# Kernel optimization log

Hardware: AMD Instinct MI355X
Metric: run time of the kernel (lower is better)

## Reference

```python
import jax, jax.numpy as jnp
import numpy as np

EPS = 1e-12  # torch F.normalize default eps


def conv1x1(x, w, b):
    # x: [N,C,H,W], w: [K,C], b: [K]
    return jnp.einsum('nchw,kc->nkhw', x, w) + b[None, :, None, None]


def forward_sa(f1, f2, cw1, cb1, cw2, cb2):
    n, _, h, w = f1.shape
    c1 = conv1x1(f1, cw1, cb1)  # [N,1,H,W]
    c2 = conv1x1(f2, cw2, cb2)
    c1 = jax.nn.softmax(c1.reshape(n, h * w), axis=1).reshape(n, 1, h, w)
    c2 = jax.nn.softmax(c2.reshape(n, h * w), axis=1).reshape(n, 1, h, w)
    return c1 * f1, c2 * f2


def l2norm_ch(x):
    # torch F.normalize(x) -> p=2 over dim=1 with eps clamp
    n = jnp.sqrt(jnp.sum(x * x, axis=1, keepdims=True))
    return x / jnp.maximum(n, EPS)


def forward_ca(f1, f2, pw1, pb1, pw2, pb2):
    N, C, H, W = f1.shape
    f1_cl = conv1x1(f1, pw1, pb1).reshape(N, -1, H * W)  # [N,Cl,HW]
    f2_cl = conv1x1(f2, pw2, pb2).reshape(N, -1, H * W)
    # A[n,p,q] = sum_c f2_cl[n,c,p] * f1_cl[n,c,q]  -> [N,HW,HW]
    A_c = jnp.tanh(jnp.einsum('ncp,ncq->npq', f2_cl, f1_cl))
    f1_v = f1.reshape(N, C, H * W)
    f2_v = f2.reshape(N, C, H * W)
    # f1_hat = f1_v @ A_c^T ; f2_hat = f2_v @ A_c
    f1_hat = jnp.einsum('ncp,nqp->ncq', f1_v, A_c).reshape(N, C, H, W)
    f2_hat = jnp.einsum('ncp,npq->ncq', f2_v, A_c).reshape(N, C, H, W)
    return l2norm_ch(f1_hat), l2norm_ch(f2_hat)


def setup_inputs() -> dict:
    key = jax.random.key(0)
    ks = jax.random.split(key, 10)
    N, C, H, W = 2, 256, 64, 64
    Cl = C // 16
    sc = 1.0 / np.sqrt(C)
    return {
        'f1': jax.random.normal(ks[0], (N, C, H, W), jnp.float32),
        'f2': jax.random.normal(ks[1], (N, C, H, W), jnp.float32),
        'pw1': jax.random.normal(ks[2], (Cl, C), jnp.float32) * sc,
        'pb1': jax.random.normal(ks[3], (Cl,), jnp.float32) * sc,
        'pw2': jax.random.normal(ks[4], (Cl, C), jnp.float32) * sc,
        'pb2': jax.random.normal(ks[5], (Cl,), jnp.float32) * sc,
        'cw1': jax.random.normal(ks[6], (1, C), jnp.float32) * sc,
        'cb1': jax.random.normal(ks[7], (1,), jnp.float32) * sc,
        'cw2': jax.random.normal(ks[8], (1, C), jnp.float32) * sc,
        'cb2': jax.random.normal(ks[9], (1,), jnp.float32) * sc,
    }


def reference(f1, f2, pw1, pb1, pw2, pb2, cw1, cb1, cw2, cb2):
    f1_1, f2_1 = forward_sa(f1, f2, cw1, cb1, cw2, cb2)
    f1_hat, f2_hat = forward_ca(f1_1, f2_1, pw1, pb1, pw2, pb2)
    fp1_hat = jax.nn.relu(f1_hat + f1)
    fp2_hat = jax.nn.relu(f2_hat + f2)
    f1_2, f2_2 = forward_sa(fp1_hat, fp2_hat, cw1, cb1, cw2, cb2)
    # Original calls forward_ca(f1_2, f2_2) again but discards the result
    # and returns (f1_2, f2_2); the dead call is omitted (identical output).
    return (f1_2, f2_2)
```

## Files before the change

kernel.cpp:

```cpp
#include <hip/hip_runtime.h>
#include <hip/hip_bf16.h>
#include <math.h>

#define N_B 2
#define C_CH 256
#define HW_SZ 4096
#define CL_CH 16

typedef __bf16 bf16x8 __attribute__((ext_vector_type(8)));
typedef float f32x4 __attribute__((ext_vector_type(4)));
typedef float f32x16 __attribute__((ext_vector_type(16)));

__device__ __forceinline__ unsigned short f2bf(float x){
  __hip_bfloat16 b = __float2bfloat16(x);
  return *reinterpret_cast<unsigned short*>(&b);
}
__device__ __forceinline__ unsigned int cvtpk(float a, float b){
  unsigned int r;
  asm("v_cvt_pk_bf16_f32 %0, %1, %2" : "=v"(r) : "v"(a), "v"(b));
  return r;
}
__device__ __forceinline__ float tanh_fast(float x){
  float e = __expf(2.0f * x);
  return fmaf(-2.0f, __builtin_amdgcn_rcpf(1.0f + e), 1.0f);
}
__device__ __forceinline__ void gload16(const void* gsrc, void* lds_dst){
  __builtin_amdgcn_global_load_lds(
      (const __attribute__((address_space(1))) unsigned int*)gsrc,
      (__attribute__((address_space(3))) unsigned int*)lds_dst, 16, 0, 0);
}

__global__ void k_conv1(const float* __restrict__ f1, const float* __restrict__ f2,
                        const float* __restrict__ w1, const float* __restrict__ w2,
                        const float* __restrict__ b1, const float* __restrict__ b2,
                        float* __restrict__ cv){
  const int i = blockIdx.z, n = blockIdx.y, t = threadIdx.x;
  const int ql = t & 63, cg = t >> 6;
  const int q = blockIdx.x * 64 + ql;
  const float* f = (i ? f2 : f1) + n * C_CH * HW_SZ;
  const float* w = i ? w2 : w1;
  __shared__ float ws[C_CH];
  __shared__ float red[4][72];
  ws[t] = w[t];
  __syncthreads();
  float acc = 0.f;
  #pragma unroll 8
  for (int c = cg * 64; c < cg * 64 + 64; ++c)
    acc += f[c * HW_SZ + q] * ws[c];
  red[cg][ql] = acc;
  __syncthreads();
  if (t < 64){
    float s = red[0][t] + red[1][t] + red[2][t] + red[3][t] + (i ? b2[0] : b1[0]);
    cv[(i * 2 + n) * HW_SZ + blockIdx.x * 64 + t] = s;
  }
}

__global__ void k_softmax(const float* __restrict__ cv, float* __restrict__ pr){
  const int r = blockIdx.x, t = threadIdx.x;
  const float* x = cv + r * HW_SZ;
  float* y = pr + r * HW_SZ;
  __shared__ float red[256];
  float v[16];
  float m = -1e30f;
  #pragma unroll
  for (int j = 0; j < 16; j++){ v[j] = x[j * 256 + t]; m = fmaxf(m, v[j]); }
  red[t] = m; __syncthreads();
  for (int s = 128; s > 0; s >>= 1){ if (t < s) red[t] = fmaxf(red[t], red[t + s]); __syncthreads(); }
  m = red[0]; __syncthreads();
  float sum = 0.f;
  #pragma unroll
  for (int j = 0; j < 16; j++){ v[j] = __expf(v[j] - m); sum += v[j]; }
  red[t] = sum; __syncthreads();
  for (int s = 128; s > 0; s >>= 1){ if (t < s) red[t] += red[t + s]; __syncthreads(); }
  const float inv = 1.0f / red[0];
  #pragma unroll
  for (int j = 0; j < 16; j++) y[j * 256 + t] = v[j] * inv;
}

__global__ void k_scale_cl(const float* __restrict__ f1, const float* __restrict__ f2,
                           const float* __restrict__ pr,
                           const float* __restrict__ pw1, const float* __restrict__ pw2,
                           const float* __restrict__ pb1, const float* __restrict__ pb2,
                           unsigned short* __restrict__ fs1, unsigned short* __restrict__ fs2,
                           unsigned short* __restrict__ clT1, unsigned short* __restrict__ clT2){
  const int i = blockIdx.z, n = blockIdx.y, t = threadIdx.x;
  const int ql = t & 63, cg = t >> 6;
  const int q = blockIdx.x * 64 + ql;
  const float* f = (i ? f2 : f1) + n * C_CH * HW_SZ;
  unsigned short* fs = (i ? fs2 : fs1) + n * C_CH * HW_SZ;
  unsigned short* clT = (i ? clT2 : clT1) + n * 32 * HW_SZ;
  const float* pw = i ? pw2 : pw1;
  const float* pb = i ? pb2 : pb1;
  __shared__ float wls[CL_CH * C_CH];
  __shared__ float red[4][CL_CH][66];
  #pragma unroll
  for (int j = 0; j < 16; j++) wls[j * 256 + t] = pw[j * 256 + t];
  __syncthreads();
  const float p = pr[(i * 2 + n) * HW_SZ + q];
  float acc[16];
  #pragma unroll
  for (int k = 0; k < 16; k++) acc[k] = 0.f;
  for (int c = cg * 64; c < cg * 64 + 64; ++c){
    float vv = f[c * HW_SZ + q] * p;
    fs[c * HW_SZ + q] = f2bf(vv);
    #pragma unroll
    for (int k = 0; k < 16; k++) acc[k] += wls[k * 256 + c] * vv;
  }
  #pragma unroll
  for (int k = 0; k < 16; k++) red[cg][k][ql] = acc[k];
  __syncthreads();
  #pragma unroll
  for (int j = 0; j < 4; j++){
    int e = j * 256 + t; int k = e >> 6, qq = e & 63;
    float s = red[0][k][qq] + red[1][k][qq] + red[2][k][qq] + red[3][k][qq] + pb[k];
    clT[(blockIdx.x * 64 + qq) * 32 + k] = f2bf(s);
  }
  if (t < 128){
    uint4 zv = {0u, 0u, 0u, 0u};
    int qq = t >> 1, half = t & 1;
    *reinterpret_cast<uint4*>(&clT[(blockIdx.x * 64 + qq) * 32 + 16 + half * 8]) = zv;
  }
}

__global__ __launch_bounds__(512, 4) void k_hat(
    const unsigned short* __restrict__ fs1, const unsigned short* __restrict__ fs2,
    const unsigned short* __restrict__ clT1, const unsigned short* __restrict__ clT2,
    float* __restrict__ hat1, float* __restrict__ hat2,
    float* __restrict__ pt1, float* __restrict__ pt2){
  const int t = threadIdx.x;
  const int bid = blockIdx.x;
  const int xcd = bid & 7, slot = bid >> 3;
  const int z = xcd >> 1;
  const int n = z & 1, i = z >> 1;
  const int x = slot * 2 + (xcd & 1);
  const int qt = x >> 1, ph = x & 1;
  const int q0 = qt * 64;
  const int pbase = ph * 2048;

  const unsigned short* fs = (i ? fs2 : fs1) + n * C_CH * HW_SZ;
  const unsigned short* uT = (i ? clT1 : clT2) + n * 32 * HW_SZ;
  const unsigned short* vT = (i ? clT2 : clT1) + n * 32 * HW_SZ;
  float* out = (ph ? (i ? pt2 : pt1) : (i ? hat2 : hat1)) + n * C_CH * HW_SZ;

  __shared__ __align__(16) unsigned short fsA[2][C_CH * 64];
  __shared__ __align__(16) unsigned short aT[2][64 * 64];

  const int wv = t >> 6, l = t & 63;
  const int g4 = l >> 4, lr16 = l & 15;
  const int g2 = l >> 5, lr32 = l & 31;

  const int pfw = wv & 3;
  const int qf0 = (wv >> 2) * 2;
  const int cblk = wv & 3, qblk = wv >> 2;

  const bf16x8 ub0 = *reinterpret_cast<const bf16x8*>(&uT[(q0 + qf0 * 16 + lr16) * 32 + g4 * 8]);
  const bf16x8 ub1 = *reinterpret_cast<const bf16x8*>(&uT[(q0 + qf0 * 16 + 16 + lr16) * 32 + g4 * 8]);

  f32x16 acc0, acc1;
  #pragma unroll
  for (int r = 0; r < 16; ++r){ acc0[r] = 0.f; acc1[r] = 0.f; }
  const f32x4 zz = {0.f, 0.f, 0.f, 0.f};

  int fs_src[4];
  #pragma unroll
  for (int it = 0; it < 4; ++it){
    int d = it * 512 + t; int c = d >> 3, sl = d & 7;
    int u = sl ^ (c & 7) ^ (((c >> 3) & 1) << 2);
    fs_src[it] = c * (HW_SZ * 2) + u * 16;
  }
  const char* vbase = (const char*)vT;
  const int vgo = (pfw * 16 + lr16) * 64 + g4 * 16;
  unsigned atw0;
  {
    int qd = qf0 * 16 + lr16;
    int sw = (pfw * 2 + (g4 >> 1)) ^ (qd & 7) ^ (((qd >> 3) & 1) << 2);
    atw0 = qd * 128 + sw * 16 + (g4 & 1) * 8;
  }
  unsigned afo[2], bqo;
  #pragma unroll
  for (int cf = 0; cf < 2; ++cf){
    int crow = cblk * 64 + cf * 32 + lr32;
    afo[cf] = crow * 128 + ((g2 ^ (crow & 7) ^ (((crow >> 3) & 1) << 2)) << 4);
  }
  {
    int qrow = qblk * 32 + lr32;
    bqo = qrow * 128 + ((g2 ^ (qrow & 7) ^ (((qrow >> 3) & 1) << 2)) << 4);
  }

  auto vload = [&](int kk) -> uint4 {
    return *reinterpret_cast<const uint4*>(vbase + (pbase + kk * 64) * 64 + vgo);
  };
  auto stage_fs = [&](unsigned short* dstbase, int p0){
    const char* src = (const char*)fs + p0 * 2;
    #pragma unroll
    for (int it = 0; it < 4; ++it)
      gload16(src + fs_src[it], dstbase + (it * 512 + wv * 64) * 8);
  };
  auto dgen = [&](uint4 vr, char* atB){
    bf16x8 av = *reinterpret_cast<bf16x8*>(&vr);
    f32x4 d0 = __builtin_amdgcn_mfma_f32_16x16x32_bf16(av, ub0, zz, 0, 0, 0);
    f32x4 d1 = __builtin_amdgcn_mfma_f32_16x16x32_bf16(av, ub1, zz, 0, 0, 0);
    uint2 pk0, pk1;
    pk0.x = cvtpk(tanh_fast(d0[0]), tanh_fast(d0[1]));
    pk0.y = cvtpk(tanh_fast(d0[2]), tanh_fast(d0[3]));
    pk1.x = cvtpk(tanh_fast(d1[0]), tanh_fast(d1[1]));
    pk1.y = cvtpk(tanh_fast(d1[2]), tanh_fast(d1[3]));
    *reinterpret_cast<uint2*>(atB + atw0) = pk0;
    *reinterpret_cast<uint2*>(atB + atw0 + 2048) = pk1;
  };
  auto mmain = [&](const char* faB, const char* atB){
    #pragma unroll
    for (int ks = 0; ks < 4; ++ks){
      unsigned kx = (unsigned)(ks << 5);
      bf16x8 b0 = *reinterpret_cast<const bf16x8*>(atB + (bqo ^ kx));
      bf16x8 a0 = *reinterpret_cast<const bf16x8*>(faB + (afo[0] ^ kx));
      bf16x8 a1 = *reinterpret_cast<const bf16x8*>(faB + (afo[1] ^ kx));
      acc0 = __builtin_amdgcn_mfma_f32_32x32x16_bf16(a0, b0, acc0, 0, 0, 0);
      acc1 = __builtin_amdgcn_mfma_f32_32x32x16_bf16(a1, b0, acc1, 0, 0, 0);
    }
  };

  uint4 va = vload(0);
  uint4 vb = vload(1);
  stage_fs(fsA[0], pbase);
  dgen(va, (char*)aT[0]);
  __syncthreads();

  #pragma unroll 1
  for (int k2 = 0; k2 < 16; ++k2){
    {
      const int k = 2 * k2;
      stage_fs(fsA[1], pbase + (k + 1) * 64);
      va = vload(k + 2);
      dgen(vb, (char*)aT[1]);
      mmain((const char*)fsA[0], (const char*)aT[0]);
      __syncthreads();
    }
    {
      const int k = 2 * k2 + 1;
      stage_fs(fsA[0], pbase + (k + 1) * 64);
      vb = vload(k + 2);
      dgen(va, (char*)aT[0]);
      mmain((const char*)fsA[1], (const char*)aT[1]);
      __syncthreads();
    }
  }

  const int qcol = q0 + qblk * 32 + lr32;
  #pragma unroll
  for (int r = 0; r < 16; ++r){
    int cr = (r & 3) + 8 * (r >> 2) + 4 * g2;
    out[(cblk * 64 + cr) * HW_SZ + qcol] = acc0[r];
    out[(cblk * 64 + 32 + cr) * HW_SZ + qcol] = acc1[r];
  }
}

__global__ void k_norm(float* __restrict__ hat1, float* __restrict__ hat2,
                       const float* __restrict__ pt1, const float* __restrict__ pt2,
                       const float* __restrict__ f1, const float* __restrict__ f2,
                       const float* __restrict__ cw1, const float* __restrict__ cw2,
                       const float* __restrict__ cb1, const float* __restrict__ cb2,
                       float* __restrict__ cv2){
  const int i = blockIdx.z, n = blockIdx.y, t = threadIdx.x;
  const int ql = t & 31, cg = t >> 5;
  const int q = blockIdx.x * 32 + ql;
  float* hat = (i ? hat2 : hat1) + n * C_CH * HW_SZ;
  const float* pt = (i ? pt2 : pt1) + n * C_CH * HW_SZ;
  const float* f = (i ? f2 : f1) + n * C_CH * HW_SZ;
  __shared__ float ws[C_CH];
  __shared__ float red[8][36];
  __shared__ float invs[32];
  ws[t] = (i ? cw2 : cw1)[t];
  __syncthreads();
  float hc[32];
  float s = 0.f;
  #pragma unroll
  for (int j = 0; j < 32; ++j){
    int c = cg * 32 + j;
    float h = hat[c * HW_SZ + q] + pt[c * HW_SZ + q];
    hc[j] = h;
    s += h * h;
  }
  red[cg][ql] = s; __syncthreads();
  if (t < 32){
    float ss = 0.f;
    #pragma unroll
    for (int g = 0; g < 8; ++g) ss += red[g][t];
    invs[t] = 1.0f / fmaxf(sqrtf(ss), 1e-12f);
  }
  __syncthreads();
  const float inv = invs[ql];
  float ca = 0.f;
  #pragma unroll
  for (int j = 0; j < 32; ++j){
    int c = cg * 32 + j;
    float vv = fmaxf(hc[j] * inv + f[c * HW_SZ + q], 0.0f);
    hat[c * HW_SZ + q] = vv;
    ca += ws[c] * vv;
  }
  red[cg][ql] = ca; __syncthreads();
  if (t < 32){
    float ss = (i ? cb2[0] : cb1[0]);
    #pragma unroll
    for (int g = 0; g < 8; ++g) ss += red[g][t];
    cv2[(i * 2 + n) * HW_SZ + blockIdx.x * 32 + t] = ss;
  }
}

__global__ void k_final(const float* __restrict__ fp1, const float* __restrict__ fp2,
                        const float* __restrict__ pr2, float* __restrict__ outp){
  const int i = blockIdx.z;
  const int idx4 = (blockIdx.x * 256 + threadIdx.x) * 4;
  const int n = idx4 >> 20;
  const int q = idx4 & (HW_SZ - 1);
  const float* fp = i ? fp2 : fp1;
  float4 vv = *reinterpret_cast<const float4*>(&fp[idx4]);
  float4 pp = *reinterpret_cast<const float4*>(&pr2[(i * 2 + n) * HW_SZ + q]);
  float4 o; o.x = vv.x * pp.x; o.y = vv.y * pp.y; o.z = vv.z * pp.z; o.w = vv.w * pp.w;
  *reinterpret_cast<float4*>(&outp[i * (C_CH * HW_SZ * N_B) + idx4]) = o;
}

extern "C" void kernel_launch(void* const* d_in, const int* in_sizes, int n_in,
                              void* d_out, int out_size, void* d_ws, size_t ws_size,
                              hipStream_t stream){
  const float* f1  = (const float*)d_in[0];
  const float* f2  = (const float*)d_in[1];
  const float* pw1 = (const float*)d_in[2];
  const float* pb1 = (const float*)d_in[3];
  const float* pw2 = (const float*)d_in[4];
  const float* pb2 = (const float*)d_in[5];
  const float* cw1 = (const float*)d_in[6];
  const float* cb1 = (const float*)d_in[7];
  const float* cw2 = (const float*)d_in[8];
  const float* cb2 = (const float*)d_in[9];
  float* ws = (float*)d_ws;
  float* HAT1 = ws;
  float* HAT2 = ws + 2097152;
  float* PT1  = ws + 4194304;
  float* PT2  = ws + 6291456;
  unsigned short* FS1 = (unsigned short*)(ws + 8388608);
  unsigned short* FS2 = (unsigned short*)(ws + 9437184);
  unsigned short* CLT1 = (unsigned short*)(ws + 10485760);
  unsigned short* CLT2 = (unsigned short*)(ws + 10616832);
  float* CV1  = ws + 10747904;
  float* PR1  = ws + 10764288;
  float* CV2  = ws + 10780672;
  float* PR2  = ws + 10797056;
  float* outp = (float*)d_out;

  k_conv1   <<<dim3(64, 2, 2), 256, 0, stream>>>(f1, f2, cw1, cw2, cb1, cb2, CV1);
  k_softmax <<<4, 256, 0, stream>>>(CV1, PR1);
  k_scale_cl<<<dim3(64, 2, 2), 256, 0, stream>>>(f1, f2, PR1, pw1, pw2, pb1, pb2,
                                                 FS1, FS2, CLT1, CLT2);
  k_hat     <<<512, 512, 0, stream>>>(FS1, FS2, CLT1, CLT2, HAT1, HAT2, PT1, PT2);
  k_norm    <<<dim3(128, 2, 2), 256, 0, stream>>>(HAT1, HAT2, PT1, PT2, f1, f2,
                                                  cw1, cw2, cb1, cb2, CV2);
  k_softmax <<<4, 256, 0, stream>>>(CV2, PR2);
  k_final   <<<dim3(2048, 1, 2), 256, 0, stream>>>(HAT1, HAT2, PR2, outp);
}
```

Measured before the change: 107.7 us.

## Widen k_hat q-tile to 128 and rework k_norm to 64-column blocks

k_hat now computes a 128-wide q tile per block with a 2x2 MFMA accumulator grid per wave, halving the grid to 256 blocks and reusing each staged fs tile across twice as many output columns. The cost being cut is the repeated global streaming of fs per q tile. In exchange the A tile in shared memory doubles, register pressure rises (launch bounds relaxed to 2), and fewer blocks are available to fill the device. k_norm switches to 64 columns per block and drops the 32-float register cache, so hat and pt are re-read from global memory in a second pass instead.

```diff
diff --git a/kernel.cpp b/kernel.cpp
--- a/kernel.cpp
+++ b/kernel.cpp
@@ -122,7 +122,7 @@
   }
 }
 
-__global__ __launch_bounds__(512, 4) void k_hat(
+__global__ __launch_bounds__(512, 2) void k_hat(
     const unsigned short* __restrict__ fs1, const unsigned short* __restrict__ fs2,
     const unsigned short* __restrict__ clT1, const unsigned short* __restrict__ clT2,
     float* __restrict__ hat1, float* __restrict__ hat2,
@@ -134,7 +134,7 @@
   const int n = z & 1, i = z >> 1;
   const int x = slot * 2 + (xcd & 1);
   const int qt = x >> 1, ph = x & 1;
-  const int q0 = qt * 64;
+  const int q0 = qt * 128;
   const int pbase = ph * 2048;
 
   const unsigned short* fs = (i ? fs2 : fs1) + n * C_CH * HW_SZ;
@@ -143,22 +143,24 @@
   float* out = (ph ? (i ? pt2 : pt1) : (i ? hat2 : hat1)) + n * C_CH * HW_SZ;
 
   __shared__ __align__(16) unsigned short fsA[2][C_CH * 64];
-  __shared__ __align__(16) unsigned short aT[2][64 * 64];
+  __shared__ __align__(16) unsigned short aT[2][128 * 64];
 
   const int wv = t >> 6, l = t & 63;
   const int g4 = l >> 4, lr16 = l & 15;
   const int g2 = l >> 5, lr32 = l & 31;
 
   const int pfw = wv & 3;
-  const int qf0 = (wv >> 2) * 2;
+  const int qh  = wv >> 2;
   const int cblk = wv & 3, qblk = wv >> 2;
 
-  const bf16x8 ub0 = *reinterpret_cast<const bf16x8*>(&uT[(q0 + qf0 * 16 + lr16) * 32 + g4 * 8]);
-  const bf16x8 ub1 = *reinterpret_cast<const bf16x8*>(&uT[(q0 + qf0 * 16 + 16 + lr16) * 32 + g4 * 8]);
-
-  f32x16 acc0, acc1;
-  #pragma unroll
-  for (int r = 0; r < 16; ++r){ acc0[r] = 0.f; acc1[r] = 0.f; }
+  bf16x8 ub[4];
+  #pragma unroll
+  for (int j = 0; j < 4; ++j)
+    ub[j] = *reinterpret_cast<const bf16x8*>(&uT[(q0 + qh * 64 + j * 16 + lr16) * 32 + g4 * 8]);
+
+  f32x16 acc00, acc01, acc10, acc11;
+  #pragma unroll
+  for (int r = 0; r < 16; ++r){ acc00[r] = 0.f; acc01[r] = 0.f; acc10[r] = 0.f; acc11[r] = 0.f; }
   const f32x4 zz = {0.f, 0.f, 0.f, 0.f};
 
   int fs_src[4];
@@ -172,19 +174,20 @@
   const int vgo = (pfw * 16 + lr16) * 64 + g4 * 16;
   unsigned atw0;
   {
-    int qd = qf0 * 16 + lr16;
+    int qd = qh * 64 + lr16;
     int sw = (pfw * 2 + (g4 >> 1)) ^ (qd & 7) ^ (((qd >> 3) & 1) << 2);
     atw0 = qd * 128 + sw * 16 + (g4 & 1) * 8;
   }
-  unsigned afo[2], bqo;
+  unsigned afo[2], bqo[2];
   #pragma unroll
   for (int cf = 0; cf < 2; ++cf){
     int crow = cblk * 64 + cf * 32 + lr32;
     afo[cf] = crow * 128 + ((g2 ^ (crow & 7) ^ (((crow >> 3) & 1) << 2)) << 4);
   }
-  {
-    int qrow = qblk * 32 + lr32;
-    bqo = qrow * 128 + ((g2 ^ (qrow & 7) ^ (((qrow >> 3) & 1) << 2)) << 4);
+  #pragma unroll
+  for (int qf = 0; qf < 2; ++qf){
+    int qrow = qblk * 64 + qf * 32 + lr32;
+    bqo[qf] = qrow * 128 + ((g2 ^ (qrow & 7) ^ (((qrow >> 3) & 1) << 2)) << 4);
   }
 
   auto vload = [&](int kk) -> uint4 {
@@ -198,25 +201,27 @@
   };
   auto dgen = [&](uint4 vr, char* atB){
     bf16x8 av = *reinterpret_cast<bf16x8*>(&vr);
-    f32x4 d0 = __builtin_amdgcn_mfma_f32_16x16x32_bf16(av, ub0, zz, 0, 0, 0);
-    f32x4 d1 = __builtin_amdgcn_mfma_f32_16x16x32_bf16(av, ub1, zz, 0, 0, 0);
-    uint2 pk0, pk1;
-    pk0.x = cvtpk(tanh_fast(d0[0]), tanh_fast(d0[1]));
-    pk0.y = cvtpk(tanh_fast(d0[2]), tanh_fast(d0[3]));
-    pk1.x = cvtpk(tanh_fast(d1[0]), tanh_fast(d1[1]));
-    pk1.y = cvtpk(tanh_fast(d1[2]), tanh_fast(d1[3]));
-    *reinterpret_cast<uint2*>(atB + atw0) = pk0;
-    *reinterpret_cast<uint2*>(atB + atw0 + 2048) = pk1;
+    #pragma unroll
+    for (int j = 0; j < 4; ++j){
+      f32x4 d = __builtin_amdgcn_mfma_f32_16x16x32_bf16(av, ub[j], zz, 0, 0, 0);
+      uint2 pk;
+      pk.x = cvtpk(tanh_fast(d[0]), tanh_fast(d[1]));
+      pk.y = cvtpk(tanh_fast(d[2]), tanh_fast(d[3]));
+      *reinterpret_cast<uint2*>(atB + atw0 + j * 2048) = pk;
+    }
   };
   auto mmain = [&](const char* faB, const char* atB){
     #pragma unroll
     for (int ks = 0; ks < 4; ++ks){
       unsigned kx = (unsigned)(ks << 5);
-      bf16x8 b0 = *reinterpret_cast<const bf16x8*>(atB + (bqo ^ kx));
       bf16x8 a0 = *reinterpret_cast<const bf16x8*>(faB + (afo[0] ^ kx));
       bf16x8 a1 = *reinterpret_cast<const bf16x8*>(faB + (afo[1] ^ kx));
-      acc0 = __builtin_amdgcn_mfma_f32_32x32x16_bf16(a0, b0, acc0, 0, 0, 0);
-      acc1 = __builtin_amdgcn_mfma_f32_32x32x16_bf16(a1, b0, acc1, 0, 0, 0);
+      bf16x8 b0 = *reinterpret_cast<const bf16x8*>(atB + (bqo[0] ^ kx));
+      bf16x8 b1 = *reinterpret_cast<const bf16x8*>(atB + (bqo[1] ^ kx));
+      acc00 = __builtin_amdgcn_mfma_f32_32x32x16_bf16(a0, b0, acc00, 0, 0, 0);
+      acc01 = __builtin_amdgcn_mfma_f32_32x32x16_bf16(a0, b1, acc01, 0, 0, 0);
+      acc10 = __builtin_amdgcn_mfma_f32_32x32x16_bf16(a1, b0, acc10, 0, 0, 0);
+      acc11 = __builtin_amdgcn_mfma_f32_32x32x16_bf16(a1, b1, acc11, 0, 0, 0);
     }
   };
 
@@ -246,12 +251,14 @@
     }
   }
 
-  const int qcol = q0 + qblk * 32 + lr32;
+  const int qcol = q0 + qblk * 64 + lr32;
   #pragma unroll
   for (int r = 0; r < 16; ++r){
     int cr = (r & 3) + 8 * (r >> 2) + 4 * g2;
-    out[(cblk * 64 + cr) * HW_SZ + qcol] = acc0[r];
-    out[(cblk * 64 + 32 + cr) * HW_SZ + qcol] = acc1[r];
+    out[(cblk * 64 + cr) * HW_SZ + qcol] = acc00[r];
+    out[(cblk * 64 + cr) * HW_SZ + qcol + 32] = acc01[r];
+    out[(cblk * 64 + 32 + cr) * HW_SZ + qcol] = acc10[r];
+    out[(cblk * 64 + 32 + cr) * HW_SZ + qcol + 32] = acc11[r];
   }
 }
 
@@ -262,48 +269,41 @@
                        const float* __restrict__ cb1, const float* __restrict__ cb2,
                        float* __restrict__ cv2){
   const int i = blockIdx.z, n = blockIdx.y, t = threadIdx.x;
-  const int ql = t & 31, cg = t >> 5;
-  const int q = blockIdx.x * 32 + ql;
+  const int ql = t & 63, cg = t >> 6;
+  const int q = blockIdx.x * 64 + ql;
   float* hat = (i ? hat2 : hat1) + n * C_CH * HW_SZ;
   const float* pt = (i ? pt2 : pt1) + n * C_CH * HW_SZ;
   const float* f = (i ? f2 : f1) + n * C_CH * HW_SZ;
   __shared__ float ws[C_CH];
-  __shared__ float red[8][36];
-  __shared__ float invs[32];
+  __shared__ float red[4][72];
+  __shared__ float invs[64];
   ws[t] = (i ? cw2 : cw1)[t];
   __syncthreads();
-  float hc[32];
   float s = 0.f;
-  #pragma unroll
-  for (int j = 0; j < 32; ++j){
-    int c = cg * 32 + j;
+  #pragma unroll 8
+  for (int c = cg * 64; c < cg * 64 + 64; ++c){
     float h = hat[c * HW_SZ + q] + pt[c * HW_SZ + q];
-    hc[j] = h;
     s += h * h;
   }
   red[cg][ql] = s; __syncthreads();
-  if (t < 32){
-    float ss = 0.f;
-    #pragma unroll
-    for (int g = 0; g < 8; ++g) ss += red[g][t];
+  if (t < 64){
+    float ss = red[0][t] + red[1][t] + red[2][t] + red[3][t];
     invs[t] = 1.0f / fmaxf(sqrtf(ss), 1e-12f);
   }
   __syncthreads();
   const float inv = invs[ql];
   float ca = 0.f;
-  #pragma unroll
-  for (int j = 0; j < 32; ++j){
-    int c = cg * 32 + j;
-    float vv = fmaxf(hc[j] * inv + f[c * HW_SZ + q], 0.0f);
+  #pragma unroll 8
+  for (int c = cg * 64; c < cg * 64 + 64; ++c){
+    float h = hat[c * HW_SZ + q] + pt[c * HW_SZ + q];
+    float vv = fmaxf(h * inv + f[c * HW_SZ + q], 0.0f);
     hat[c * HW_SZ + q] = vv;
     ca += ws[c] * vv;
   }
   red[cg][ql] = ca; __syncthreads();
-  if (t < 32){
-    float ss = (i ? cb2[0] : cb1[0]);
-    #pragma unroll
-    for (int g = 0; g < 8; ++g) ss += red[g][t];
-    cv2[(i * 2 + n) * HW_SZ + blockIdx.x * 32 + t] = ss;
+  if (t < 64){
+    float ss = red[0][t] + red[1][t] + red[2][t] + red[3][t] + (i ? cb2[0] : cb1[0]);
+    cv2[(i * 2 + n) * HW_SZ + blockIdx.x * 64 + t] = ss;
   }
 }
 
@@ -352,9 +352,9 @@
   k_softmax <<<4, 256, 0, stream>>>(CV1, PR1);
   k_scale_cl<<<dim3(64, 2, 2), 256, 0, stream>>>(f1, f2, PR1, pw1, pw2, pb1, pb2,
                                                  FS1, FS2, CLT1, CLT2);
-  k_hat     <<<512, 512, 0, stream>>>(FS1, FS2, CLT1, CLT2, HAT1, HAT2, PT1, PT2);
-  k_norm    <<<dim3(128, 2, 2), 256, 0, stream>>>(HAT1, HAT2, PT1, PT2, f1, f2,
-                                                  cw1, cw2, cb1, cb2, CV2);
+  k_hat     <<<256, 512, 0, stream>>>(FS1, FS2, CLT1, CLT2, HAT1, HAT2, PT1, PT2);
+  k_norm    <<<dim3(64, 2, 2), 256, 0, stream>>>(HAT1, HAT2, PT1, PT2, f1, f2,
+                                                 cw1, cw2, cb1, cb2, CV2);
   k_softmax <<<4, 256, 0, stream>>>(CV2, PR2);
   k_final   <<<dim3(2048, 1, 2), 256, 0, stream>>>(HAT1, HAT2, PR2, outp);
 }
```

New measurement: 105.4 us. -2.2%, faster.
